# Kernel optimization log

Measured on AMD Instinct MI355X. Metric: run time of the kernel, lower is better.

Reference implementation:

```python
import jax, jax.numpy as jnp
import numpy as np
import math

D_MODEL = 1024
N_HEADS = 16
HEAD_DIM = D_MODEL // N_HEADS


def setup_inputs() -> dict:
    key = jax.random.key(0)
    ks = jax.random.split(key, 6)
    scale = 1.0 / math.sqrt(D_MODEL)
    x = jax.random.normal(ks[0], (4, 2048, D_MODEL), dtype=jnp.float32)
    # nn.Linear weights stored as [out, in]; we keep [in, out] for x @ W
    Wq = jax.random.uniform(ks[1], (D_MODEL, D_MODEL), jnp.float32, -scale, scale)
    Wk = jax.random.uniform(ks[2], (D_MODEL, D_MODEL), jnp.float32, -scale, scale)
    Wv = jax.random.uniform(ks[3], (D_MODEL, D_MODEL), jnp.float32, -scale, scale)
    Wo = jax.random.uniform(ks[4], (D_MODEL, D_MODEL), jnp.float32, -scale, scale)
    bo = jax.random.uniform(ks[5], (D_MODEL,), jnp.float32, -scale, scale)
    return {"x": x, "Wq": Wq, "Wk": Wk, "Wv": Wv, "Wo": Wo, "bo": bo}


def reference(x, Wq, Wk, Wv, Wo, bo):
    B, S, _ = x.shape
    H, Dh = N_HEADS, HEAD_DIM
    # project and split heads -> [B, H, S, Dh]
    q = (x @ Wq).reshape(B, S, H, Dh).transpose(0, 2, 1, 3)
    k = (x @ Wk).reshape(B, S, H, Dh).transpose(0, 2, 1, 3)
    v = (x @ Wv).reshape(B, S, H, Dh).transpose(0, 2, 1, 3)
    scores = jnp.einsum('bhqd,bhkd->bhqk', q, k) / math.sqrt(Dh)
    causal = jnp.tril(jnp.ones((S, S), dtype=bool))  # True = keep
    scores = jnp.where(causal, scores, -jnp.inf)
    attn = jax.nn.softmax(scores, axis=-1)  # dropout=0.0 -> no-op
    out = jnp.einsum('bhqk,bhkd->bhqd', attn, v)
    out = out.transpose(0, 2, 1, 3).reshape(B, S, H * Dh)
    return out @ Wo + bo
```

## Files before the change

kernel.cpp:

```cpp
#include <hip/hip_runtime.h>
#include <hip/hip_bf16.h>

#define DEV __device__ __forceinline__

typedef unsigned short u16;
typedef unsigned int u32;
typedef __bf16 bf16x8 __attribute__((ext_vector_type(8)));
typedef float f32x4 __attribute__((ext_vector_type(4)));

static constexpr int S   = 2048;
static constexpr int D   = 1024;
static constexpr int H   = 16;
static constexpr int Dh  = 64;
static constexpr int B_  = 4;
static constexpr int M   = B_ * S;

DEV u16 f2bf(float f) {
    __hip_bfloat16 h = __float2bfloat16(f);
    union { __hip_bfloat16 h; u16 u; } cv; cv.h = h; return cv.u;
}
DEV float bf2f(u16 u) {
    union { u16 u; __hip_bfloat16 h; } cv; cv.u = u; return __bfloat162float(cv.h);
}
DEV f32x4 mfma16(bf16x8 a, bf16x8 b, f32x4 c) {
    return __builtin_amdgcn_mfma_f32_16x16x32_bf16(a, b, c, 0, 0, 0);
}
DEV void llds16(const u16* g, u16* l) {
    __builtin_amdgcn_global_load_lds(
        (const __attribute__((address_space(1))) u32*)g,
        (__attribute__((address_space(3))) u32*)l, 16, 0, 0);
}
DEV bf16x8 ld8f(const float* p) {
    const f32x4* q = reinterpret_cast<const f32x4*>(p);
    f32x4 a = q[0], b = q[1];
    union { u16 u[8]; bf16x8 v; } r;
    r.u[0] = f2bf(a[0]); r.u[1] = f2bf(a[1]); r.u[2] = f2bf(a[2]); r.u[3] = f2bf(a[3]);
    r.u[4] = f2bf(b[0]); r.u[5] = f2bf(b[1]); r.u[6] = f2bf(b[2]); r.u[7] = f2bf(b[3]);
    return r.v;
}

__global__ __launch_bounds__(256) void x_to_bf16(
    const float* __restrict__ x, u16* __restrict__ xb)
{
    size_t i = ((size_t)blockIdx.x * 256 + threadIdx.x) * 8;
    *reinterpret_cast<bf16x8*>(xb + i) = ld8f(x + i);
}

__global__ __launch_bounds__(256) void transpose_w(
    const float* __restrict__ Wq, const float* __restrict__ Wk,
    const float* __restrict__ Wv, const float* __restrict__ Wo,
    u16* __restrict__ WT)
{
    const float* src = blockIdx.z == 0 ? Wq : blockIdx.z == 1 ? Wk
                     : blockIdx.z == 2 ? Wv : Wo;
    u16* dst = WT + (size_t)blockIdx.z * D * D;
    __shared__ u16 T[64 * 72];
    const int k0 = blockIdx.x * 64, n0 = blockIdx.y * 64;
    const int tid = threadIdx.x;
    for (int c = tid; c < 512; c += 256) {
        int r = c >> 3, cc = (c & 7) << 3;
        *reinterpret_cast<bf16x8*>(&T[r * 72 + cc]) =
            ld8f(&src[(size_t)(k0 + r) * D + n0 + cc]);
    }
    __syncthreads();
    for (int c = tid; c < 512; c += 256) {
        int r = c >> 3, cc = (c & 7) << 3;
        u16 tmp[8];
        #pragma unroll
        for (int i = 0; i < 8; ++i) tmp[i] = T[(cc + i) * 72 + r];
        *reinterpret_cast<bf16x8*>(&dst[(size_t)(n0 + r) * D + k0 + cc]) =
            *reinterpret_cast<const bf16x8*>(tmp);
    }
}

__global__ __launch_bounds__(256) void qkv_gemm128(
    const u16* __restrict__ A, const u16* __restrict__ WT,
    u16* __restrict__ qkv)
{
    const int bm = blockIdx.x;
    const int bn = blockIdx.y;

    __shared__ u16 As[128 * 32];
    __shared__ u16 Bs[128 * 32];

    const int tid  = threadIdx.x;
    const int wave = tid >> 6, ln = tid & 63;
    const int ln15 = ln & 15, quad = ln >> 4;
    const int wm = (wave >> 1) * 64, wn = (wave & 1) * 64;

    const u16* Ab = A  + (size_t)(bm * 128) * D;
    const u16* Bb = WT + (size_t)(bn * 128) * D;

    const int c0  = wave * 128 + ln;
    const int c1  = c0 + 64;
    const int r0  = c0 >> 2, o0 = (c0 & 3) * 8;
    const int r1  = c1 >> 2, o1 = (c1 & 3) * 8;

    f32x4 acc[4][4] = {};

    for (int k0 = 0; k0 < D; k0 += 32) {
        __syncthreads();
        llds16(Ab + (size_t)r0 * D + k0 + o0, &As[(wave * 2 + 0) * 512]);
        llds16(Ab + (size_t)r1 * D + k0 + o1, &As[(wave * 2 + 1) * 512]);
        llds16(Bb + (size_t)r0 * D + k0 + o0, &Bs[(wave * 2 + 0) * 512]);
        llds16(Bb + (size_t)r1 * D + k0 + o1, &Bs[(wave * 2 + 1) * 512]);
        __syncthreads();
        bf16x8 af[4], bfr[4];
        #pragma unroll
        for (int i = 0; i < 4; ++i)
            af[i] = *reinterpret_cast<const bf16x8*>(&As[(wm + i * 16 + ln15) * 32 + quad * 8]);
        #pragma unroll
        for (int j = 0; j < 4; ++j)
            bfr[j] = *reinterpret_cast<const bf16x8*>(&Bs[(wn + j * 16 + ln15) * 32 + quad * 8]);
        #pragma unroll
        for (int i = 0; i < 4; ++i)
            #pragma unroll
            for (int j = 0; j < 4; ++j)
                acc[i][j] = mfma16(af[i], bfr[j], acc[i][j]);
    }

    const int matn = bn >> 3;
    u16* outp = qkv + (size_t)matn * M * D;
    #pragma unroll
    for (int i = 0; i < 4; ++i)
        #pragma unroll
        for (int j = 0; j < 4; ++j)
            #pragma unroll
            for (int r = 0; r < 4; ++r) {
                int t = bm * 128 + wm + i * 16 + quad * 4 + r;
                int b = t >> 11, s = t & (S - 1);
                int n = (bn & 7) * 128 + wn + j * 16 + ln15;
                int head = n >> 6, dh = n & 63;
                outp[(((size_t)(b * H + head)) * S + s) * Dh + dh] = f2bf(acc[i][j][r]);
            }
}

__global__ __launch_bounds__(256) void vt_transpose(
    const u16* __restrict__ v, u16* __restrict__ vtout)
{
    const int st = blockIdx.x;
    const int bh = blockIdx.y;
    __shared__ u16 T[64 * 72];
    const u16* src = v + ((size_t)bh * S + st * 64) * Dh;
    u16* dst = vtout + (size_t)bh * Dh * S + st * 64;
    const int tid = threadIdx.x;
    for (int c = tid; c < 512; c += 256) {
        int r = c >> 3, cc = (c & 7) << 3;
        *reinterpret_cast<bf16x8*>(&T[r * 72 + cc]) =
            *reinterpret_cast<const bf16x8*>(&src[r * 64 + cc]);
    }
    __syncthreads();
    for (int c = tid; c < 512; c += 256) {
        int r = c >> 3, cc = (c & 7) << 3;
        u16 tmp[8];
        #pragma unroll
        for (int i = 0; i < 8; ++i) tmp[i] = T[(cc + i) * 72 + r];
        *reinterpret_cast<bf16x8*>(&dst[(size_t)r * S + cc]) =
            *reinterpret_cast<const bf16x8*>(tmp);
    }
}

__global__ __launch_bounds__(256) void attn_kernel(
    const u16* __restrict__ qbuf, const u16* __restrict__ kbuf,
    const u16* __restrict__ vt, u16* __restrict__ attno)
{
    const int i  = blockIdx.x;
    const int bh = blockIdx.y;
    const int b = bh >> 4, h = bh & 15;
    const int qt[4] = {i, 15 - i, 16 + i, 31 - i};

    __shared__ u16 Ks[64 * 64];
    __shared__ u16 Vs[64 * 64];
    __shared__ u16 Ps[4][16 * 72];

    const int tid  = threadIdx.x;
    const int wave = tid >> 6, ln = tid & 63;
    const int ln15 = ln & 15, quad = ln >> 4;
    const int swz  = ln15 & 7;

    const u16* kp0 = kbuf + (size_t)bh * S * Dh;
    const u16* vp0 = vt   + (size_t)bh * Dh * S;

    bf16x8 qf[4][2];
    #pragma unroll
    for (int t = 0; t < 4; ++t) {
        const u16* qp = qbuf + ((size_t)bh * S + qt[t] * 64) * Dh;
        for (int c = tid; c < 512; c += 256) {
            int r = c >> 3, cc = (c & 7) << 3;
            *reinterpret_cast<bf16x8*>(&Ks[r * 64 + cc]) =
                *reinterpret_cast<const bf16x8*>(&qp[r * 64 + cc]);
        }
        __syncthreads();
        #pragma unroll
        for (int st = 0; st < 2; ++st) {
            union { bf16x8 v; u16 u[8]; } in, ot;
            in.v = *reinterpret_cast<const bf16x8*>(&Ks[(wave * 16 + ln15) * 64 + st * 32 + quad * 8]);
            #pragma unroll
            for (int k = 0; k < 8; ++k) ot.u[k] = f2bf(bf2f(in.u[k]) * 0.18033688f);
            qf[t][st] = ot.v;
        }
        __syncthreads();
    }

    float l_st[4][4] = {};
    f32x4 o_st[4][4] = {};

    u16* psw = &Ps[wave][0];
    const int lrow = wave * 16 + quad * 4;

    auto step = [&](int t, bool domask) {
        const bf16x8* qa = qf[t];
        float* l_r = l_st[t];
        f32x4* oa = o_st[t];
        f32x4 sf[4] = {};
        #pragma unroll
        for (int j = 0; j < 4; ++j) {
            bf16x8 k0 = *reinterpret_cast<const bf16x8*>(
                &Ks[(j * 16 + ln15) * 64 + ((0 * 4 + quad) ^ swz) * 8]);
            bf16x8 k1 = *reinterpret_cast<const bf16x8*>(
                &Ks[(j * 16 + ln15) * 64 + ((1 * 4 + quad) ^ swz) * 8]);
            sf[j] = mfma16(qa[0], k0, sf[j]);
            sf[j] = mfma16(qa[1], k1, sf[j]);
        }
        if (domask) {
            #pragma unroll
            for (int j = 0; j < 4; ++j) {
                int kg = j * 16 + ln15;
                #pragma unroll
                for (int r = 0; r < 4; ++r)
                    if (kg > lrow + r) sf[j][r] = -3e38f;
            }
        }
        #pragma unroll
        for (int j = 0; j < 4; ++j)
            #pragma unroll
            for (int r = 0; r < 4; ++r) {
                float p = exp2f(sf[j][r] - 24.0f);
                sf[j][r] = p;
                l_r[r] += p;
            }
        #pragma unroll
        for (int j = 0; j < 4; ++j)
            #pragma unroll
            for (int r = 0; r < 4; ++r)
                psw[(quad * 4 + r) * 72 + j * 16 + ln15] = f2bf(sf[j][r]);

        #pragma unroll
        for (int st = 0; st < 2; ++st) {
            bf16x8 pa = *reinterpret_cast<const bf16x8*>(&psw[ln15 * 72 + st * 32 + quad * 8]);
            #pragma unroll
            for (int jd = 0; jd < 4; ++jd) {
                bf16x8 vv = *reinterpret_cast<const bf16x8*>(
                    &Vs[(jd * 16 + ln15) * 64 + ((st * 4 + quad) ^ swz) * 8]);
                oa[jd] = mfma16(pa, vv, oa[jd]);
            }
        }
    };

    const int c0 = wave * 128 + ln;
    const int c1 = c0 + 64;
    const int kr0 = c0 >> 3, ko0 = (((c0 & 7) ^ (kr0 & 7)) * 8);
    const int kr1 = c1 >> 3, ko1 = (((c1 & 7) ^ (kr1 & 7)) * 8);

    const int nstage = qt[3] + 1;
    for (int kblk = 0; kblk < nstage; ++kblk) {
        __syncthreads();
        llds16(kp0 + ((size_t)kblk * 64 + kr0) * Dh + ko0, &Ks[(wave * 2 + 0) * 512]);
        llds16(kp0 + ((size_t)kblk * 64 + kr1) * Dh + ko1, &Ks[(wave * 2 + 1) * 512]);
        llds16(vp0 + (size_t)kr0 * S + kblk * 64 + ko0,    &Vs[(wave * 2 + 0) * 512]);
        llds16(vp0 + (size_t)kr1 * S + kblk * 64 + ko1,    &Vs[(wave * 2 + 1) * 512]);
        __syncthreads();
        step(3, kblk == qt[3]);
        if (kblk <= qt[2]) step(2, kblk == qt[2]);
        if (kblk <= qt[1]) step(1, kblk == qt[1]);
        if (kblk <= qt[0]) step(0, kblk == qt[0]);
    }

    #pragma unroll
    for (int t = 0; t < 4; ++t) {
        float linv[4];
        #pragma unroll
        for (int r = 0; r < 4; ++r) {
            float l = l_st[t][r];
            l += __shfl_xor(l, 1, 64);
            l += __shfl_xor(l, 2, 64);
            l += __shfl_xor(l, 4, 64);
            l += __shfl_xor(l, 8, 64);
            linv[r] = 1.0f / l;
        }
        #pragma unroll
        for (int jd = 0; jd < 4; ++jd)
            #pragma unroll
            for (int r = 0; r < 4; ++r) {
                int qrow = qt[t] * 64 + wave * 16 + quad * 4 + r;
                size_t off = ((size_t)(b * S + qrow)) * D + h * Dh + jd * 16 + ln15;
                attno[off] = f2bf(o_st[t][jd][r] * linv[r]);
            }
    }
}

__global__ __launch_bounds__(256) void proj_gemm128(
    const u16* __restrict__ A, const u16* __restrict__ WoT,
    const float* __restrict__ bo, float* __restrict__ out)
{
    const int bm = blockIdx.x;
    const int bn = blockIdx.y;

    __shared__ u16 As[128 * 32];
    __shared__ u16 Bs[128 * 32];

    const int tid  = threadIdx.x;
    const int wave = tid >> 6, ln = tid & 63;
    const int ln15 = ln & 15, quad = ln >> 4;
    const int wm = (wave >> 1) * 64, wn = (wave & 1) * 64;

    const u16* Ab = A   + (size_t)(bm * 128) * D;
    const u16* Bb = WoT + (size_t)(bn * 128) * D;

    const int c0 = wave * 128 + ln;
    const int c1 = c0 + 64;
    const int r0 = c0 >> 2, o0 = (c0 & 3) * 8;
    const int r1 = c1 >> 2, o1 = (c1 & 3) * 8;

    f32x4 acc[4][4] = {};

    for (int k0 = 0; k0 < D; k0 += 32) {
        __syncthreads();
        llds16(Ab + (size_t)r0 * D + k0 + o0, &As[(wave * 2 + 0) * 512]);
        llds16(Ab + (size_t)r1 * D + k0 + o1, &As[(wave * 2 + 1) * 512]);
        llds16(Bb + (size_t)r0 * D + k0 + o0, &Bs[(wave * 2 + 0) * 512]);
        llds16(Bb + (size_t)r1 * D + k0 + o1, &Bs[(wave * 2 + 1) * 512]);
        __syncthreads();
        bf16x8 af[4], bfr[4];
        #pragma unroll
        for (int i = 0; i < 4; ++i)
            af[i] = *reinterpret_cast<const bf16x8*>(&As[(wm + i * 16 + ln15) * 32 + quad * 8]);
        #pragma unroll
        for (int j = 0; j < 4; ++j)
            bfr[j] = *reinterpret_cast<const bf16x8*>(&Bs[(wn + j * 16 + ln15) * 32 + quad * 8]);
        #pragma unroll
        for (int i = 0; i < 4; ++i)
            #pragma unroll
            for (int j = 0; j < 4; ++j)
                acc[i][j] = mfma16(af[i], bfr[j], acc[i][j]);
    }

    #pragma unroll
    for (int i = 0; i < 4; ++i)
        #pragma unroll
        for (int j = 0; j < 4; ++j)
            #pragma unroll
            for (int r = 0; r < 4; ++r) {
                int t   = bm * 128 + wm + i * 16 + quad * 4 + r;
                int col = bn * 128 + wn + j * 16 + ln15;
                out[(size_t)t * D + col] = acc[i][j][r] + bo[col];
            }
}

extern "C" void kernel_launch(void* const* d_in, const int* in_sizes, int n_in,
                              void* d_out, int out_size, void* d_ws, size_t ws_size,
                              hipStream_t stream) {
    const float* x  = (const float*)d_in[0];
    const float* Wq = (const float*)d_in[1];
    const float* Wk = (const float*)d_in[2];
    const float* Wv = (const float*)d_in[3];
    const float* Wo = (const float*)d_in[4];
    const float* bo = (const float*)d_in[5];
    float* out = (float*)d_out;
    u16* ws  = (u16*)d_ws;

    u16* WT   = ws;
    u16* xb   = WT + (size_t)4 * D * D;
    u16* qkvb = xb + (size_t)M * D;
    u16* kb   = qkvb + (size_t)M * D;
    u16* vb   = qkvb + (size_t)2 * M * D;
    u16* vtb  = xb;
    u16* attn = vb;

    x_to_bf16   <<<dim3(M * D / (256 * 8)), 256, 0, stream>>>(x, xb);
    transpose_w <<<dim3(16, 16, 4), 256, 0, stream>>>(Wq, Wk, Wv, Wo, WT);
    qkv_gemm128 <<<dim3(64, 24),    256, 0, stream>>>(xb, WT, qkvb);
    vt_transpose<<<dim3(32, 64),    256, 0, stream>>>(vb, vtb);
    attn_kernel <<<dim3(8, 64),     256, 0, stream>>>(qkvb, kb, vtb, attn);
    proj_gemm128<<<dim3(64, 8),     256, 0, stream>>>(attn, WT + (size_t)3 * D * D, bo, out);
}
```

Before: 281.1 us.

## Fuse V transpose into QKV GEMM epilogue and double-buffer attention K/V tiles

The QKV GEMM now writes the V projection directly in transposed layout through a shared-memory staging tile, which removes the separate vt_transpose kernel and its extra read and write of V. The attention kernel double-buffers the K/V shared tiles, issuing the next block's async loads before computing the current one. It also hoists the K/V fragment reads into registers once per block, shared across the four query tiles. This adds shared memory and register pressure, which could lower occupancy.

```diff
diff --git a/kernel.cpp b/kernel.cpp
--- a/kernel.cpp
+++ b/kernel.cpp
@@ -75,13 +75,14 @@
 
 __global__ __launch_bounds__(256) void qkv_gemm128(
     const u16* __restrict__ A, const u16* __restrict__ WT,
-    u16* __restrict__ qkv)
+    u16* __restrict__ qkv, u16* __restrict__ vtb)
 {
     const int bm = blockIdx.x;
     const int bn = blockIdx.y;
 
     __shared__ u16 As[128 * 32];
     __shared__ u16 Bs[128 * 32];
+    __shared__ u16 Tt[64 * 136];
 
     const int tid  = threadIdx.x;
     const int wave = tid >> 6, ln = tid & 63;
@@ -120,43 +121,46 @@
     }
 
     const int matn = bn >> 3;
-    u16* outp = qkv + (size_t)matn * M * D;
-    #pragma unroll
-    for (int i = 0; i < 4; ++i)
-        #pragma unroll
-        for (int j = 0; j < 4; ++j)
-            #pragma unroll
-            for (int r = 0; r < 4; ++r) {
-                int t = bm * 128 + wm + i * 16 + quad * 4 + r;
-                int b = t >> 11, s = t & (S - 1);
-                int n = (bn & 7) * 128 + wn + j * 16 + ln15;
-                int head = n >> 6, dh = n & 63;
-                outp[(((size_t)(b * H + head)) * S + s) * Dh + dh] = f2bf(acc[i][j][r]);
-            }
-}
-
-__global__ __launch_bounds__(256) void vt_transpose(
-    const u16* __restrict__ v, u16* __restrict__ vtout)
-{
-    const int st = blockIdx.x;
-    const int bh = blockIdx.y;
-    __shared__ u16 T[64 * 72];
-    const u16* src = v + ((size_t)bh * S + st * 64) * Dh;
-    u16* dst = vtout + (size_t)bh * Dh * S + st * 64;
-    const int tid = threadIdx.x;
-    for (int c = tid; c < 512; c += 256) {
-        int r = c >> 3, cc = (c & 7) << 3;
-        *reinterpret_cast<bf16x8*>(&T[r * 72 + cc]) =
-            *reinterpret_cast<const bf16x8*>(&src[r * 64 + cc]);
-    }
-    __syncthreads();
-    for (int c = tid; c < 512; c += 256) {
-        int r = c >> 3, cc = (c & 7) << 3;
-        u16 tmp[8];
-        #pragma unroll
-        for (int i = 0; i < 8; ++i) tmp[i] = T[(cc + i) * 72 + r];
-        *reinterpret_cast<bf16x8*>(&dst[(size_t)r * S + cc]) =
-            *reinterpret_cast<const bf16x8*>(tmp);
+    if (matn < 2) {
+        u16* outp = qkv + (size_t)matn * M * D;
+        #pragma unroll
+        for (int i = 0; i < 4; ++i)
+            #pragma unroll
+            for (int j = 0; j < 4; ++j)
+                #pragma unroll
+                for (int r = 0; r < 4; ++r) {
+                    int t = bm * 128 + wm + i * 16 + quad * 4 + r;
+                    int b = t >> 11, s = t & (S - 1);
+                    int n = (bn & 7) * 128 + wn + j * 16 + ln15;
+                    int head = n >> 6, dh = n & 63;
+                    outp[(((size_t)(b * H + head)) * S + s) * Dh + dh] = f2bf(acc[i][j][r]);
+                }
+    } else {
+        const int t0 = bm * 128, b = t0 >> 11, s0 = t0 & (S - 1);
+        #pragma unroll
+        for (int h2 = 0; h2 < 2; ++h2) {
+            __syncthreads();
+            if ((wn == 0) == (h2 == 0)) {
+                #pragma unroll
+                for (int i = 0; i < 4; ++i)
+                    #pragma unroll
+                    for (int j = 0; j < 4; ++j)
+                        #pragma unroll
+                        for (int r = 0; r < 4; ++r) {
+                            int sl = wm + i * 16 + quad * 4 + r;
+                            int dh = j * 16 + ln15;
+                            Tt[dh * 136 + sl] = f2bf(acc[i][j][r]);
+                        }
+            }
+            __syncthreads();
+            const int bh = b * H + (bn & 7) * 2 + h2;
+            u16* dst = vtb + (size_t)bh * Dh * S + s0;
+            for (int c = tid; c < 1024; c += 256) {
+                int r = c >> 4, cc = (c & 15) * 8;
+                *reinterpret_cast<bf16x8*>(&dst[(size_t)r * S + cc]) =
+                    *reinterpret_cast<const bf16x8*>(&Tt[r * 136 + cc]);
+            }
+        }
     }
 }
 
@@ -169,8 +173,8 @@
     const int b = bh >> 4, h = bh & 15;
     const int qt[4] = {i, 15 - i, 16 + i, 31 - i};
 
-    __shared__ u16 Ks[64 * 64];
-    __shared__ u16 Vs[64 * 64];
+    __shared__ u16 Ks[2][64 * 64];
+    __shared__ u16 Vs[2][64 * 64];
     __shared__ u16 Ps[4][16 * 72];
 
     const int tid  = threadIdx.x;
@@ -187,14 +191,14 @@
         const u16* qp = qbuf + ((size_t)bh * S + qt[t] * 64) * Dh;
         for (int c = tid; c < 512; c += 256) {
             int r = c >> 3, cc = (c & 7) << 3;
-            *reinterpret_cast<bf16x8*>(&Ks[r * 64 + cc]) =
+            *reinterpret_cast<bf16x8*>(&Ks[0][r * 64 + cc]) =
                 *reinterpret_cast<const bf16x8*>(&qp[r * 64 + cc]);
         }
         __syncthreads();
         #pragma unroll
         for (int st = 0; st < 2; ++st) {
             union { bf16x8 v; u16 u[8]; } in, ot;
-            in.v = *reinterpret_cast<const bf16x8*>(&Ks[(wave * 16 + ln15) * 64 + st * 32 + quad * 8]);
+            in.v = *reinterpret_cast<const bf16x8*>(&Ks[0][(wave * 16 + ln15) * 64 + st * 32 + quad * 8]);
             #pragma unroll
             for (int k = 0; k < 8; ++k) ot.u[k] = f2bf(bf2f(in.u[k]) * 0.18033688f);
             qf[t][st] = ot.v;
@@ -207,6 +211,20 @@
 
     u16* psw = &Ps[wave][0];
     const int lrow = wave * 16 + quad * 4;
+
+    const int c0 = wave * 128 + ln;
+    const int c1 = c0 + 64;
+    const int kr0 = c0 >> 3, ko0 = (((c0 & 7) ^ (kr0 & 7)) * 8);
+    const int kr1 = c1 >> 3, ko1 = (((c1 & 7) ^ (kr1 & 7)) * 8);
+
+    auto stage = [&](int kblk, int buf) {
+        llds16(kp0 + ((size_t)kblk * 64 + kr0) * Dh + ko0, &Ks[buf][(wave * 2 + 0) * 512]);
+        llds16(kp0 + ((size_t)kblk * 64 + kr1) * Dh + ko1, &Ks[buf][(wave * 2 + 1) * 512]);
+        llds16(vp0 + (size_t)kr0 * S + kblk * 64 + ko0,    &Vs[buf][(wave * 2 + 0) * 512]);
+        llds16(vp0 + (size_t)kr1 * S + kblk * 64 + ko1,    &Vs[buf][(wave * 2 + 1) * 512]);
+    };
+
+    bf16x8 kf[2][4], vf[2][4];
 
     auto step = [&](int t, bool domask) {
         const bf16x8* qa = qf[t];
@@ -215,12 +233,8 @@
         f32x4 sf[4] = {};
         #pragma unroll
         for (int j = 0; j < 4; ++j) {
-            bf16x8 k0 = *reinterpret_cast<const bf16x8*>(
-                &Ks[(j * 16 + ln15) * 64 + ((0 * 4 + quad) ^ swz) * 8]);
-            bf16x8 k1 = *reinterpret_cast<const bf16x8*>(
-                &Ks[(j * 16 + ln15) * 64 + ((1 * 4 + quad) ^ swz) * 8]);
-            sf[j] = mfma16(qa[0], k0, sf[j]);
-            sf[j] = mfma16(qa[1], k1, sf[j]);
+            sf[j] = mfma16(qa[0], kf[0][j], sf[j]);
+            sf[j] = mfma16(qa[1], kf[1][j], sf[j]);
         }
         if (domask) {
             #pragma unroll
@@ -249,31 +263,31 @@
         for (int st = 0; st < 2; ++st) {
             bf16x8 pa = *reinterpret_cast<const bf16x8*>(&psw[ln15 * 72 + st * 32 + quad * 8]);
             #pragma unroll
-            for (int jd = 0; jd < 4; ++jd) {
-                bf16x8 vv = *reinterpret_cast<const bf16x8*>(
-                    &Vs[(jd * 16 + ln15) * 64 + ((st * 4 + quad) ^ swz) * 8]);
-                oa[jd] = mfma16(pa, vv, oa[jd]);
-            }
+            for (int jd = 0; jd < 4; ++jd)
+                oa[jd] = mfma16(pa, vf[st][jd], oa[jd]);
         }
     };
 
-    const int c0 = wave * 128 + ln;
-    const int c1 = c0 + 64;
-    const int kr0 = c0 >> 3, ko0 = (((c0 & 7) ^ (kr0 & 7)) * 8);
-    const int kr1 = c1 >> 3, ko1 = (((c1 & 7) ^ (kr1 & 7)) * 8);
-
     const int nstage = qt[3] + 1;
+    stage(0, 0);
+    int cur = 0;
     for (int kblk = 0; kblk < nstage; ++kblk) {
         __syncthreads();
-        llds16(kp0 + ((size_t)kblk * 64 + kr0) * Dh + ko0, &Ks[(wave * 2 + 0) * 512]);
-        llds16(kp0 + ((size_t)kblk * 64 + kr1) * Dh + ko1, &Ks[(wave * 2 + 1) * 512]);
-        llds16(vp0 + (size_t)kr0 * S + kblk * 64 + ko0,    &Vs[(wave * 2 + 0) * 512]);
-        llds16(vp0 + (size_t)kr1 * S + kblk * 64 + ko1,    &Vs[(wave * 2 + 1) * 512]);
-        __syncthreads();
+        if (kblk + 1 < nstage) stage(kblk + 1, cur ^ 1);
+        #pragma unroll
+        for (int st = 0; st < 2; ++st)
+            #pragma unroll
+            for (int j = 0; j < 4; ++j) {
+                kf[st][j] = *reinterpret_cast<const bf16x8*>(
+                    &Ks[cur][(j * 16 + ln15) * 64 + ((st * 4 + quad) ^ swz) * 8]);
+                vf[st][j] = *reinterpret_cast<const bf16x8*>(
+                    &Vs[cur][(j * 16 + ln15) * 64 + ((st * 4 + quad) ^ swz) * 8]);
+            }
         step(3, kblk == qt[3]);
         if (kblk <= qt[2]) step(2, kblk == qt[2]);
         if (kblk <= qt[1]) step(1, kblk == qt[1]);
         if (kblk <= qt[0]) step(0, kblk == qt[0]);
+        cur ^= 1;
     }
 
     #pragma unroll
@@ -373,14 +387,12 @@
     u16* xb   = WT + (size_t)4 * D * D;
     u16* qkvb = xb + (size_t)M * D;
     u16* kb   = qkvb + (size_t)M * D;
-    u16* vb   = qkvb + (size_t)2 * M * D;
-    u16* vtb  = xb;
-    u16* attn = vb;
+    u16* vtb  = qkvb + (size_t)2 * M * D;
+    u16* attn = xb;
 
     x_to_bf16   <<<dim3(M * D / (256 * 8)), 256, 0, stream>>>(x, xb);
     transpose_w <<<dim3(16, 16, 4), 256, 0, stream>>>(Wq, Wk, Wv, Wo, WT);
-    qkv_gemm128 <<<dim3(64, 24),    256, 0, stream>>>(xb, WT, qkvb);
-    vt_transpose<<<dim3(32, 64),    256, 0, stream>>>(vb, vtb);
+    qkv_gemm128 <<<dim3(64, 24),    256, 0, stream>>>(xb, WT, qkvb, vtb);
     attn_kernel <<<dim3(8, 64),     256, 0, stream>>>(qkvb, kb, vtb, attn);
     proj_gemm128<<<dim3(64, 8),     256, 0, stream>>>(attn, WT + (size_t)3 * D * D, bo, out);
 }
```

Result: no change. 280.3 us (-0.3%).
